# Kernel optimization log

Hardware: AMD Instinct MI355X
Metric: run time of the kernel (lower is better)

The kernel has to match this reference:

```python
import jax, jax.numpy as jnp
import numpy as np

# dims: N batch, C channels, T frames, V=25 source joints, VP=20 target joints,
# S=3 subsets, IC=64 inter channels (out_channels // coff_embedding)
N, C, T, V, VP, S, IC = 16, 256, 256, 25, 20, 3, 64
BN_EPS = 1e-5


def setup_inputs() -> dict:
    key = jax.random.key(0)
    ks = jax.random.split(key, 14)
    s = 0.05
    return {
        "x": jax.random.normal(ks[0], (N, C, T, V), dtype=jnp.float32),
        "PA": jax.random.normal(ks[1], (S, VP, VP), dtype=jnp.float32) * 1e-3,
        "A_fix": jax.random.normal(ks[2], (S, VP, VP), dtype=jnp.float32) * s,
        "w_e": jax.random.normal(ks[3], (V, VP), dtype=jnp.float32) * s,   # ConvTranspose2d 1x1 over node dim
        "b_e": jax.random.normal(ks[4], (VP,), dtype=jnp.float32) * s,
        "wa": jax.random.normal(ks[5], (S, IC, C), dtype=jnp.float32) * s,
        "ba": jax.random.normal(ks[6], (S, IC), dtype=jnp.float32) * s,
        "wb": jax.random.normal(ks[7], (S, IC, C), dtype=jnp.float32) * s,
        "bb": jax.random.normal(ks[8], (S, IC), dtype=jnp.float32) * s,
        "wd": jax.random.normal(ks[9], (S, C, C), dtype=jnp.float32) * s,  # conv_d: in C -> out C
        "bd": jax.random.normal(ks[10], (S, C), dtype=jnp.float32) * s,
        "gamma": 1.0 + jax.random.normal(ks[11], (C,), dtype=jnp.float32) * 0.1,
        "beta": jax.random.normal(ks[12], (C,), dtype=jnp.float32) * 0.1,
    }


def reference(x, PA, A_fix, w_e, b_e, wa, ba, wb, bb, wd, bd, gamma, beta):
    n, c, t, v = x.shape
    vp = w_e.shape[1]
    s_, ic = wa.shape[0], wa.shape[1]
    # conv_e: 1x1 ConvTranspose over node axis V -> VP (bias per target node)
    xp = jnp.einsum('nctv,vu->nctu', x, w_e) + b_e            # (N,C,T,VP)
    A = A_fix + PA                                            # (S,VP,VP)
    # conv_a / conv_b for all subsets at once (1x1 convs == channel GEMMs)
    fa = jnp.einsum('nctv,sic->nsitv', xp, wa) + ba[None, :, :, None, None]  # (N,S,IC,T,VP)
    fb = jnp.einsum('nctv,sic->nsitv', xp, wb) + bb[None, :, :, None, None]
    A1 = fa.transpose(0, 1, 4, 2, 3).reshape(n, s_, vp, ic * t)   # (N,S,VP,IC*T)
    A2 = fb.reshape(n, s_, ic * t, vp)                             # (N,S,IC*T,VP)
    scores = jnp.einsum('nsvk,nsku->nsvu', A1, A2) / (ic * t)      # (N,S,VP,VP)
    att = jax.nn.softmax(scores, axis=-2) + A[None]                # softmax over dim -2, as in torch
    # x @ att per subset, then conv_d, accumulated across subsets
    z = jnp.einsum('nkv,nsvu->nsku', xp.reshape(n, c * t, vp), att)
    z = z.reshape(n, s_, c, t, vp)                                 # (N,S,C,T,VP)
    y = jnp.einsum('nsctv,soc->notv', z, wd) + bd.sum(0)[None, :, None, None]
    # BatchNorm2d (training mode: batch statistics, biased variance)
    mean = y.mean(axis=(0, 2, 3), keepdims=True)
    var = y.var(axis=(0, 2, 3), keepdims=True)
    yn = (y - mean) / jnp.sqrt(var + BN_EPS) * gamma[None, :, None, None] + beta[None, :, None, None]
    # in_channels == out_channels -> down is identity; residual uses node-remapped x
    return jax.nn.relu(yn + xp)
```

## Files before the change

kernel.cpp:

```cpp
#include <hip/hip_runtime.h>

typedef unsigned short u16;
typedef unsigned int u32;
typedef float __attribute__((ext_vector_type(4))) f32x4;
typedef short __attribute__((ext_vector_type(8))) s16x8;

#define N_ 16
#define C_ 256
#define T_ 256
#define V_ 25
#define VP_ 20
#define S_ 3
#define IC_ 64
#define M_ (T_*VP_)
#define WROWS 1152

__device__ __forceinline__ u16 f2bf(float f) {
    u32 u = __float_as_uint(f);
    u32 r = (u + 0x7FFFu + ((u >> 16) & 1u)) >> 16;
    return (u16)r;
}
__device__ __forceinline__ float bf2f(u16 h) {
    return __uint_as_float(((u32)h) << 16);
}

__global__ __launch_bounds__(256) void k_conv_e(const float* __restrict__ x,
    const float* __restrict__ w_e, const float* __restrict__ b_e, u16* __restrict__ xp)
{
    __shared__ __align__(16) float sw[V_*VP_];
    __shared__ float sb[VP_];
    int tid = threadIdx.x;
    for (int i = tid; i < V_*VP_; i += 256) sw[i] = w_e[i];
    if (tid < VP_) sb[tid] = b_e[tid];
    __syncthreads();
    long row = (long)blockIdx.x*256 + tid;
    const float* xr = x + row*V_;
    float acc[VP_];
    #pragma unroll
    for (int u = 0; u < VP_; u++) acc[u] = sb[u];
    #pragma unroll
    for (int v = 0; v < V_; v++) {
        float xv = xr[v];
        const float4* w4 = (const float4*)&sw[v*VP_];
        #pragma unroll
        for (int q = 0; q < 5; q++) {
            float4 w = w4[q];
            acc[4*q+0] = fmaf(xv, w.x, acc[4*q+0]);
            acc[4*q+1] = fmaf(xv, w.y, acc[4*q+1]);
            acc[4*q+2] = fmaf(xv, w.z, acc[4*q+2]);
            acc[4*q+3] = fmaf(xv, w.w, acc[4*q+3]);
        }
    }
    u32 ub[10];
    #pragma unroll
    for (int q = 0; q < 10; q++)
        ub[q] = (u32)f2bf(acc[2*q]) | ((u32)f2bf(acc[2*q+1]) << 16);
    uint2* o2 = (uint2*)(xp + row*VP_);
    #pragma unroll
    for (int q = 0; q < 5; q++) o2[q] = make_uint2(ub[2*q], ub[2*q+1]);
}

__global__ void k_packW(const float* __restrict__ wa, const float* __restrict__ wb,
    const float* __restrict__ wd, const float* __restrict__ ba, const float* __restrict__ bb,
    u16* __restrict__ Wb, float* __restrict__ biasv)
{
    int row = blockIdx.x, c = threadIdx.x;
    const float* src = (row < 192) ? (wa + (long)row*C_)
                     : (row < 384) ? (wb + (long)(row-192)*C_)
                                   : (wd + (long)(row-384)*C_);
    Wb[(long)row*C_ + c] = f2bf(src[c]);
    if (c == 0) biasv[row] = (row < 192) ? ba[row] : ((row < 384) ? bb[row-192] : 0.f);
}

__global__ __launch_bounds__(256) void k_tr(const u16* __restrict__ xp, u16* __restrict__ xpT)
{
    __shared__ __align__(16) u16 tile[64*68];
    int bid = blockIdx.x;
    int cb = bid & 3, mb = (bid >> 2) % 80, n = bid / 320;
    int c0 = cb*64, m0 = mb*64;
    int tid = threadIdx.x;
    int rr = tid >> 4;
    int q4 = (tid & 15) * 4;
    const u16* xin = xp + (long)n*C_*M_;
    #pragma unroll
    for (int p = 0; p < 4; p++) {
        int c = p*16 + rr;
        uint2 rv = *(const uint2*)(xin + (long)(c0+c)*M_ + m0 + q4);
        *(uint2*)(&tile[c*68 + q4]) = rv;
    }
    __syncthreads();
    u16* xout = xpT + (long)n*M_*C_;
    #pragma unroll
    for (int p = 0; p < 4; p++) {
        int m = p*16 + rr;
        u32 u0 = (u32)tile[(q4+0)*68 + m] | ((u32)tile[(q4+1)*68 + m] << 16);
        u32 u1 = (u32)tile[(q4+2)*68 + m] | ((u32)tile[(q4+3)*68 + m] << 16);
        *(uint2*)(xout + (long)(m0+m)*C_ + c0 + q4) = make_uint2(u0, u1);
    }
}

__global__ __launch_bounds__(256) void k_gemm(const u16* __restrict__ Wb,
    const u16* __restrict__ xpT, const float* __restrict__ biasv, u16* __restrict__ out)
{
    __shared__ __align__(16) short smem[128*64 + 128*64];
    short* As = smem;
    short* Bs = smem + 128*64;
    int bid = blockIdx.x;
    int nb = bid % 40;
    int mb = (bid / 40) % 9;
    int n  = bid / 360;
    int tid = threadIdx.x;
    int wid = tid >> 6, lane = tid & 63;
    int wr = wid >> 1, wc = wid & 1;

    float biasr[4][4];
    {
        int rbase = mb*128 + wr*64 + ((lane >> 4) << 2);
        #pragma unroll
        for (int m = 0; m < 4; m++)
            #pragma unroll
            for (int r = 0; r < 4; r++)
                biasr[m][r] = biasv[rbase + m*16 + r];
    }
    const u16* Ag = Wb + (long)mb*128*C_;
    const u16* Bg = xpT + ((long)n*M_ + (long)nb*128)*C_;

    f32x4 acc[4][4];
    #pragma unroll
    for (int m = 0; m < 4; m++)
        #pragma unroll
        for (int nf = 0; nf < 4; nf++)
            acc[m][nf] = f32x4{0.f, 0.f, 0.f, 0.f};

    auto stage = [&](int k0) {
        #pragma unroll
        for (int j = 0; j < 4; j++) {
            int L = j*256 + wid*64 + lane;
            int row = L >> 3, ko = (L & 7) * 8;
            __builtin_amdgcn_global_load_lds(
                (const unsigned int*)(Ag + (long)row*C_ + k0 + ko),
                (unsigned int*)(As + (j*256 + wid*64)*8), 16, 0, 0);
            __builtin_amdgcn_global_load_lds(
                (const unsigned int*)(Bg + (long)row*C_ + k0 + ko),
                (unsigned int*)(Bs + (j*256 + wid*64)*8), 16, 0, 0);
        }
    };

    stage(0);
    __syncthreads();
    for (int kt = 0; kt < 4; kt++) {
        #pragma unroll
        for (int ks = 0; ks < 2; ks++) {
            s16x8 af[4], bg[4];
            #pragma unroll
            for (int m = 0; m < 4; m++)
                af[m] = *(const s16x8*)(As + (wr*64 + m*16 + (lane & 15))*64 + ks*32 + ((lane >> 4) << 3));
            #pragma unroll
            for (int nf = 0; nf < 4; nf++)
                bg[nf] = *(const s16x8*)(Bs + (wc*64 + nf*16 + (lane & 15))*64 + ks*32 + ((lane >> 4) << 3));
            #pragma unroll
            for (int m = 0; m < 4; m++)
                #pragma unroll
                for (int nf = 0; nf < 4; nf++)
                    acc[m][nf] = __builtin_amdgcn_mfma_f32_16x16x32_bf16(af[m], bg[nf], acc[m][nf], 0, 0, 0);
        }
        if (kt < 3) {
            __syncthreads();
            stage((kt+1)*64);
            __syncthreads();
        }
    }
    __syncthreads();
    u16* Cs = (u16*)smem;
    #pragma unroll
    for (int m = 0; m < 4; m++)
        #pragma unroll
        for (int nf = 0; nf < 4; nf++)
            #pragma unroll
            for (int r = 0; r < 4; r++) {
                int row = wr*64 + m*16 + ((lane >> 4) << 2) + r;
                int col = wc*64 + nf*16 + (lane & 15);
                Cs[row*128 + col] = f2bf(acc[m][nf][r] + biasr[m][r]);
            }
    __syncthreads();
    u16* og = out + ((long)n*WROWS + (long)mb*128)*M_ + (long)nb*128;
    #pragma unroll
    for (int j = 0; j < 8; j++) {
        int idx = j*256 + tid;
        int row = idx >> 4, c8 = (idx & 15) * 8;
        uint4 v = *(const uint4*)(Cs + row*128 + c8);
        *(uint4*)(og + (long)row*M_ + c8) = v;
    }
}

__global__ __launch_bounds__(256) void k_scores_mfma(const u16* __restrict__ fafbg,
    float* __restrict__ scores)
{
    __shared__ __align__(16) u16 sfa[2*256*VP_];
    __shared__ __align__(16) u16 sfb[2*256*VP_];
    __shared__ float ssc[VP_*VP_];
    int bid = blockIdx.x;
    int kc = bid & 31;
    int s  = (bid >> 5) % 3;
    int n  = bid / 96;
    int tid = threadIdx.x;
    int w = tid >> 6, lane = tid & 63;

    const uint4* fa4 = (const uint4*)(fafbg + ((long)n*WROWS + s*IC_ + 2*kc)*M_);
    const uint4* fb4 = (const uint4*)(fafbg + ((long)n*WROWS + 192 + s*IC_ + 2*kc)*M_);
    uint4* da = (uint4*)sfa;
    uint4* db = (uint4*)sfb;
    #pragma unroll
    for (int j = 0; j < 5; j++) {
        da[j*256 + tid] = fa4[j*256 + tid];
        db[j*256 + tid] = fb4[j*256 + tid];
    }
    for (int i = tid; i < VP_*VP_; i += 256) ssc[i] = 0.f;
    __syncthreads();

    int iw = w >> 1;
    int t0 = (w & 1) * 128;
    const u16* pa = sfa + iw*256*VP_;
    const u16* pb = sfb + iw*256*VP_;
    int vrow = lane & 15;
    int kg = lane >> 4;
    f32x4 acc[2][2];
    #pragma unroll
    for (int m = 0; m < 2; m++)
        #pragma unroll
        for (int nn = 0; nn < 2; nn++)
            acc[m][nn] = f32x4{0.f, 0.f, 0.f, 0.f};

    for (int step = 0; step < 4; step++) {
        int tb = t0 + step*32 + kg*8;
        s16x8 af0, af1, bg0, bg1;
        #pragma unroll
        for (int j = 0; j < 8; j++) {
            int t = tb + j;
            af0[j] = (short)pa[t*VP_ + vrow];
            bg0[j] = (short)pb[t*VP_ + vrow];
            af1[j] = (vrow < 4) ? (short)pa[t*VP_ + 16 + vrow] : (short)0;
            bg1[j] = (vrow < 4) ? (short)pb[t*VP_ + 16 + vrow] : (short)0;
        }
        acc[0][0] = __builtin_amdgcn_mfma_f32_16x16x32_bf16(af0, bg0, acc[0][0], 0, 0, 0);
        acc[0][1] = __builtin_amdgcn_mfma_f32_16x16x32_bf16(af0, bg1, acc[0][1], 0, 0, 0);
        acc[1][0] = __builtin_amdgcn_mfma_f32_16x16x32_bf16(af1, bg0, acc[1][0], 0, 0, 0);
        acc[1][1] = __builtin_amdgcn_mfma_f32_16x16x32_bf16(af1, bg1, acc[1][1], 0, 0, 0);
    }
    #pragma unroll
    for (int m = 0; m < 2; m++)
        #pragma unroll
        for (int nn = 0; nn < 2; nn++)
            #pragma unroll
            for (int r = 0; r < 4; r++) {
                int v = m*16 + kg*4 + r;
                int u = nn*16 + vrow;
                if (v < VP_ && u < VP_)
                    atomicAdd(&ssc[v*VP_ + u], acc[m][nn][r]);
            }
    __syncthreads();
    float* scb = scores + (long)(n*S_ + s)*VP_*VP_;
    for (int i = tid; i < VP_*VP_; i += 256)
        atomicAdd(&scb[i], ssc[i]);
}

__global__ void k_att(const float* __restrict__ scores, const float* __restrict__ PA,
    const float* __restrict__ A_fix, float* __restrict__ att)
{
    int ns = blockIdx.x;
    int s = ns - (ns / S_)*S_;
    int u = threadIdx.x;
    if (u >= VP_) return;
    const float* sc = scores + (long)ns*VP_*VP_;
    const float inv = 1.0f / (IC_*T_);
    float m = -1e30f;
    for (int v = 0; v < VP_; v++) m = fmaxf(m, sc[v*VP_+u]);
    m *= inv;
    float e[VP_]; float sum = 0.f;
    for (int v = 0; v < VP_; v++) { float t = __expf(sc[v*VP_+u]*inv - m); e[v] = t; sum += t; }
    float r = 1.0f / sum;
    const float* Ab = A_fix + s*VP_*VP_;
    const float* Pb = PA    + s*VP_*VP_;
    float* ob = att + (long)ns*VP_*VP_;
    for (int v = 0; v < VP_; v++) ob[v*VP_+u] = e[v]*r + Ab[v*VP_+u] + Pb[v*VP_+u];
}

__global__ __launch_bounds__(128) void k_comb(const u16* __restrict__ fafbg,
    const float* __restrict__ att, const float* __restrict__ bd, float* __restrict__ out)
{
    __shared__ __align__(16) u16 gsh[S_*C_*VP_];
    __shared__ __align__(16) float attsh[S_*VP_*VP_];
    int nt = blockIdx.x, n = nt >> 8, t = nt & 255;
    int tid = threadIdx.x;
    for (int i = tid; i < S_*VP_*VP_; i += 128) attsh[i] = att[(long)n*S_*VP_*VP_ + i];
    const u32* gbase = (const u32*)fafbg;
    u32* gsh32 = (u32*)gsh;
    for (int j = 0; j < 60; j++) {
        int idx = j*128 + tid;
        int r = idx / 10, d = idx - r*10;
        gsh32[idx] = gbase[(long)(n*WROWS + 384 + r)*2560 + t*10 + d];
    }
    __syncthreads();
    int o0 = tid, o1 = tid + 128;
    float acc0[VP_], acc1[VP_];
    {
        float bs0 = bd[o0] + bd[C_+o0] + bd[2*C_+o0];
        float bs1 = bd[o1] + bd[C_+o1] + bd[2*C_+o1];
        #pragma unroll
        for (int u = 0; u < VP_; u++) { acc0[u] = bs0; acc1[u] = bs1; }
    }
    for (int s = 0; s < S_; s++) {
        #pragma unroll
        for (int v = 0; v < VP_; v++) {
            const float4* ar = (const float4*)&attsh[(s*VP_+v)*VP_];
            float g0 = bf2f(gsh[(s*C_+o0)*VP_ + v]);
            float g1 = bf2f(gsh[(s*C_+o1)*VP_ + v]);
            #pragma unroll
            for (int q = 0; q < 5; q++) {
                float4 a = ar[q];
                acc0[4*q+0] = fmaf(g0, a.x, acc0[4*q+0]);
                acc0[4*q+1] = fmaf(g0, a.y, acc0[4*q+1]);
                acc0[4*q+2] = fmaf(g0, a.z, acc0[4*q+2]);
                acc0[4*q+3] = fmaf(g0, a.w, acc0[4*q+3]);
                acc1[4*q+0] = fmaf(g1, a.x, acc1[4*q+0]);
                acc1[4*q+1] = fmaf(g1, a.y, acc1[4*q+1]);
                acc1[4*q+2] = fmaf(g1, a.z, acc1[4*q+2]);
                acc1[4*q+3] = fmaf(g1, a.w, acc1[4*q+3]);
            }
        }
    }
    float4* y0 = (float4*)(out + (((long)n*C_ + o0)*T_ + t)*VP_);
    float4* y1 = (float4*)(out + (((long)n*C_ + o1)*T_ + t)*VP_);
    #pragma unroll
    for (int q = 0; q < 5; q++) {
        y0[q] = make_float4(acc0[4*q], acc0[4*q+1], acc0[4*q+2], acc0[4*q+3]);
        y1[q] = make_float4(acc1[4*q], acc1[4*q+1], acc1[4*q+2], acc1[4*q+3]);
    }
}

__global__ __launch_bounds__(256) void k_bnstat(const float* __restrict__ y,
    const float* __restrict__ gamma, const float* __restrict__ beta,
    float* __restrict__ scale, float* __restrict__ shift)
{
    int o = blockIdx.x, tid = threadIdx.x;
    float sum = 0.f, sq = 0.f;
    for (int n = 0; n < N_; n++) {
        const float4* p = (const float4*)(y + (long)(n*C_ + o)*T_*VP_);
        for (int idx = tid; idx < T_*VP_/4; idx += 256) {
            float4 v = p[idx];
            sum += v.x + v.y + v.z + v.w;
            sq  += v.x*v.x + v.y*v.y + v.z*v.z + v.w*v.w;
        }
    }
    __shared__ float s1[256], s2[256];
    s1[tid] = sum; s2[tid] = sq;
    __syncthreads();
    for (int off = 128; off > 0; off >>= 1) {
        if (tid < off) { s1[tid] += s1[tid+off]; s2[tid] += s2[tid+off]; }
        __syncthreads();
    }
    if (tid == 0) {
        const float M = (float)(N_*T_*VP_);
        float mean = s1[0] / M;
        float var  = s2[0] / M - mean*mean;
        float g = gamma[o] * rsqrtf(var + 1e-5f);
        scale[o] = g;
        shift[o] = beta[o] - mean*g;
    }
}

__global__ void k_final(float* __restrict__ out, const u16* __restrict__ xp,
    const float* __restrict__ scale, const float* __restrict__ shift)
{
    const long total4 = (long)N_*C_*T_*VP_/4;
    long stride = (long)gridDim.x * blockDim.x;
    for (long i4 = (long)blockIdx.x*blockDim.x + threadIdx.x; i4 < total4; i4 += stride) {
        int c = (int)((i4 / (T_*VP_/4)) & (C_-1));
        float4 v = ((const float4*)out)[i4];
        uint2 xu = ((const uint2*)xp)[i4];
        float sc = scale[c], sh = shift[c];
        float x0 = __uint_as_float(xu.x << 16);
        float x1 = __uint_as_float(xu.x & 0xFFFF0000u);
        float x2 = __uint_as_float(xu.y << 16);
        float x3 = __uint_as_float(xu.y & 0xFFFF0000u);
        v.x = fmaxf(fmaf(v.x, sc, sh) + x0, 0.f);
        v.y = fmaxf(fmaf(v.y, sc, sh) + x1, 0.f);
        v.z = fmaxf(fmaf(v.z, sc, sh) + x2, 0.f);
        v.w = fmaxf(fmaf(v.w, sc, sh) + x3, 0.f);
        ((float4*)out)[i4] = v;
    }
}

extern "C" void kernel_launch(void* const* d_in, const int* in_sizes, int n_in,
                              void* d_out, int out_size, void* d_ws, size_t ws_size,
                              hipStream_t stream)
{
    const float* x     = (const float*)d_in[0];
    const float* PA    = (const float*)d_in[1];
    const float* A_fix = (const float*)d_in[2];
    const float* w_e   = (const float*)d_in[3];
    const float* b_e   = (const float*)d_in[4];
    const float* wa    = (const float*)d_in[5];
    const float* ba    = (const float*)d_in[6];
    const float* wb    = (const float*)d_in[7];
    const float* bb    = (const float*)d_in[8];
    const float* wd    = (const float*)d_in[9];
    const float* bd    = (const float*)d_in[10];
    const float* gamma = (const float*)d_in[11];
    const float* beta  = (const float*)d_in[12];
    float* out = (float*)d_out;

    char* ws = (char*)d_ws;
    const size_t FAFBG_B = (size_t)N_*WROWS*M_*2;
    const size_t XP_B    = (size_t)N_*C_*T_*VP_*2;
    const size_t WB_B    = (size_t)WROWS*C_*2;
    const size_t BIAS_B  = (size_t)WROWS*4;
    const size_t SC_B    = (size_t)N_*S_*VP_*VP_*4;
    u16*   fafbg = (u16*)(ws);
    u16*   xp    = (u16*)(ws + FAFBG_B);
    u16*   xpT   = (u16*)(ws + FAFBG_B + XP_B);
    u16*   Wb    = (u16*)(ws + FAFBG_B + 2*XP_B);
    float* biasv = (float*)(ws + FAFBG_B + 2*XP_B + WB_B);
    float* scores= (float*)(ws + FAFBG_B + 2*XP_B + WB_B + BIAS_B);
    float* att   = (float*)(ws + FAFBG_B + 2*XP_B + WB_B + BIAS_B + SC_B);
    float* scale = (float*)(ws + FAFBG_B + 2*XP_B + WB_B + BIAS_B + 2*SC_B);
    float* shift = scale + C_;

    k_conv_e<<<4096, 256, 0, stream>>>(x, w_e, b_e, xp);
    k_packW<<<WROWS, 256, 0, stream>>>(wa, wb, wd, ba, bb, Wb, biasv);
    k_tr<<<5120, 256, 0, stream>>>(xp, xpT);
    k_gemm<<<5760, 256, 0, stream>>>(Wb, xpT, biasv, fafbg);
    hipMemsetAsync(scores, 0, SC_B, stream);
    k_scores_mfma<<<N_*S_*32, 256, 0, stream>>>(fafbg, scores);
    k_att<<<N_*S_, 32, 0, stream>>>(scores, PA, A_fix, att);
    k_comb<<<4096, 128, 0, stream>>>(fafbg, att, bd, out);
    k_bnstat<<<C_, 256, 0, stream>>>(out, gamma, beta, scale, shift);
    k_final<<<2048, 256, 0, stream>>>(out, xp, scale, shift);
}
```

Baseline: 550.3 us.

## Remap k_comb to one block per (n,channel) with direct coalesced g loads

k_comb now assigns one block per batch and output channel and one thread per frame, instead of one block per (batch, frame). Each thread reads its 20 bf16 g values for each subset directly from global memory as contiguous vectors, so the large shared-memory staging of g goes away. Output rows are written contiguously across threads. This targets poorly coalesced strided reads and writes and the heavy LDS footprint that limited occupancy. The trade-off is less reuse of the att tile per block and more blocks re-loading it.

```diff
diff --git a/kernel.cpp b/kernel.cpp
--- a/kernel.cpp
+++ b/kernel.cpp
@@ -285,57 +285,52 @@
     for (int v = 0; v < VP_; v++) ob[v*VP_+u] = e[v]*r + Ab[v*VP_+u] + Pb[v*VP_+u];
 }
 
-__global__ __launch_bounds__(128) void k_comb(const u16* __restrict__ fafbg,
+__global__ __launch_bounds__(256) void k_comb(const u16* __restrict__ fafbg,
     const float* __restrict__ att, const float* __restrict__ bd, float* __restrict__ out)
 {
-    __shared__ __align__(16) u16 gsh[S_*C_*VP_];
     __shared__ __align__(16) float attsh[S_*VP_*VP_];
-    int nt = blockIdx.x, n = nt >> 8, t = nt & 255;
-    int tid = threadIdx.x;
-    for (int i = tid; i < S_*VP_*VP_; i += 128) attsh[i] = att[(long)n*S_*VP_*VP_ + i];
-    const u32* gbase = (const u32*)fafbg;
-    u32* gsh32 = (u32*)gsh;
-    for (int j = 0; j < 60; j++) {
-        int idx = j*128 + tid;
-        int r = idx / 10, d = idx - r*10;
-        gsh32[idx] = gbase[(long)(n*WROWS + 384 + r)*2560 + t*10 + d];
-    }
-    __syncthreads();
-    int o0 = tid, o1 = tid + 128;
-    float acc0[VP_], acc1[VP_];
-    {
-        float bs0 = bd[o0] + bd[C_+o0] + bd[2*C_+o0];
-        float bs1 = bd[o1] + bd[C_+o1] + bd[2*C_+o1];
-        #pragma unroll
-        for (int u = 0; u < VP_; u++) { acc0[u] = bs0; acc1[u] = bs1; }
-    }
+    int bid = blockIdx.x;
+    int n = bid >> 8, o = bid & 255;
+    int t = threadIdx.x;
+    for (int i = t; i < S_*VP_*VP_; i += 256) attsh[i] = att[(long)n*S_*VP_*VP_ + i];
+    __syncthreads();
+
+    float acc[VP_];
+    float bs = bd[o] + bd[C_+o] + bd[2*C_+o];
+    #pragma unroll
+    for (int u = 0; u < VP_; u++) acc[u] = bs;
+
+    const u16* gbase = fafbg + ((long)n*WROWS + 384 + o)*M_ + t*VP_;
+    #pragma unroll
     for (int s = 0; s < S_; s++) {
+        const uint2* g2 = (const uint2*)(gbase + (long)s*C_*M_);
+        uint2 gv[5];
+        #pragma unroll
+        for (int q = 0; q < 5; q++) gv[q] = g2[q];
+        float gf[VP_];
+        #pragma unroll
+        for (int q = 0; q < 5; q++) {
+            gf[4*q+0] = bf2f((u16)gv[q].x); gf[4*q+1] = bf2f((u16)(gv[q].x >> 16));
+            gf[4*q+2] = bf2f((u16)gv[q].y); gf[4*q+3] = bf2f((u16)(gv[q].y >> 16));
+        }
         #pragma unroll
         for (int v = 0; v < VP_; v++) {
             const float4* ar = (const float4*)&attsh[(s*VP_+v)*VP_];
-            float g0 = bf2f(gsh[(s*C_+o0)*VP_ + v]);
-            float g1 = bf2f(gsh[(s*C_+o1)*VP_ + v]);
+            float g0 = gf[v];
             #pragma unroll
             for (int q = 0; q < 5; q++) {
                 float4 a = ar[q];
-                acc0[4*q+0] = fmaf(g0, a.x, acc0[4*q+0]);
-                acc0[4*q+1] = fmaf(g0, a.y, acc0[4*q+1]);
-                acc0[4*q+2] = fmaf(g0, a.z, acc0[4*q+2]);
-                acc0[4*q+3] = fmaf(g0, a.w, acc0[4*q+3]);
-                acc1[4*q+0] = fmaf(g1, a.x, acc1[4*q+0]);
-                acc1[4*q+1] = fmaf(g1, a.y, acc1[4*q+1]);
-                acc1[4*q+2] = fmaf(g1, a.z, acc1[4*q+2]);
-                acc1[4*q+3] = fmaf(g1, a.w, acc1[4*q+3]);
+                acc[4*q+0] = fmaf(g0, a.x, acc[4*q+0]);
+                acc[4*q+1] = fmaf(g0, a.y, acc[4*q+1]);
+                acc[4*q+2] = fmaf(g0, a.z, acc[4*q+2]);
+                acc[4*q+3] = fmaf(g0, a.w, acc[4*q+3]);
             }
         }
     }
-    float4* y0 = (float4*)(out + (((long)n*C_ + o0)*T_ + t)*VP_);
-    float4* y1 = (float4*)(out + (((long)n*C_ + o1)*T_ + t)*VP_);
-    #pragma unroll
-    for (int q = 0; q < 5; q++) {
-        y0[q] = make_float4(acc0[4*q], acc0[4*q+1], acc0[4*q+2], acc0[4*q+3]);
-        y1[q] = make_float4(acc1[4*q], acc1[4*q+1], acc1[4*q+2], acc1[4*q+3]);
-    }
+    float4* yb = (float4*)(out + (((long)n*C_ + o)*T_ + t)*VP_);
+    #pragma unroll
+    for (int q = 0; q < 5; q++)
+        yb[q] = make_float4(acc[4*q], acc[4*q+1], acc[4*q+2], acc[4*q+3]);
 }
 
 __global__ __launch_bounds__(256) void k_bnstat(const float* __restrict__ y,
@@ -433,7 +428,7 @@
     hipMemsetAsync(scores, 0, SC_B, stream);
     k_scores_mfma<<<N_*S_*32, 256, 0, stream>>>(fafbg, scores);
     k_att<<<N_*S_, 32, 0, stream>>>(scores, PA, A_fix, att);
-    k_comb<<<4096, 128, 0, stream>>>(fafbg, att, bd, out);
+    k_comb<<<N_*C_, 256, 0, stream>>>(fafbg, att, bd, out);
     k_bnstat<<<C_, 256, 0, stream>>>(out, gamma, beta, scale, shift);
     k_final<<<2048, 256, 0, stream>>>(out, xp, scale, shift);
 }
```

Result: faster. 444.0 us (-19.3%).
